# Kernel tuning notes

Measured on AMD Instinct MI355X. Metric: run time of the kernel, lower is better.

Reference implementation:

```python
import jax, jax.numpy as jnp
import numpy as np

# Fixed problem sizes (match input_specs): B graphs of N points each, kNN with K neighbors.
B, N, K = 32, 2048, 20
F_IN, H, C = 3, 64, 40
BN = B * N
E = BN * K


def mlp(x, w1, b1, w2, b2):
    # PyG MLP([in, H, H]) with plain last layer: Lin -> ReLU -> Lin
    return jax.nn.relu(x @ w1 + b1) @ w2 + b2


def edge_conv(x, src, dst, w1, b1, w2, b2):
    # EdgeConv message for edge j->i: MLP(cat[x_i, x_j - x_i]); aggr='max' at target i.
    xi = x[dst]                      # [E, F]
    xj = x[src]                      # [E, F]
    msg = mlp(jnp.concatenate([xi, xj - xi], axis=-1), w1, b1, w2, b2)  # [E, H]
    out = jax.ops.segment_max(msg, dst, num_segments=x.shape[0])        # [BN, H]
    # nodes with no incoming edges: -inf -> 0 (torch_scatter max fill behavior)
    return jnp.where(jnp.isfinite(out), out, jnp.zeros((), out.dtype))


def dynamic_edge_conv(x, w1, b1, w2, b2):
    # Rebuild kNN graph from current features within each graph, then EdgeConv(max).
    xb = x.reshape(B, N, -1)                                   # [B, N, H]
    sq = jnp.sum(xb * xb, axis=-1)                             # [B, N]
    # squared euclidean distances [B, N, N]
    d = sq[:, :, None] - 2.0 * jnp.einsum('bnh,bmh->bnm', xb, xb) + sq[:, None, :]
    _, idx = jax.lax.top_k(-d, K)                              # [B, N, K] nearest (incl. self)
    xj = jax.vmap(lambda xg, ig: xg[ig])(xb, idx)              # [B, N, K, H]
    xi = jnp.broadcast_to(xb[:, :, None, :], xj.shape)         # [B, N, K, H]
    msg = mlp(jnp.concatenate([xi, xj - xi], axis=-1), w1, b1, w2, b2)  # [B, N, K, H]
    return jnp.max(msg, axis=2).reshape(BN, -1)                # exactly K msgs per node


def _lin_init(key, fan_in, fan_out):
    k1, k2 = jax.random.split(key)
    s = 1.0 / np.sqrt(fan_in)
    w = jax.random.uniform(k1, (fan_in, fan_out), jnp.float32, -s, s)
    b = jax.random.uniform(k2, (fan_out,), jnp.float32, -s, s)
    return w, b


def setup_inputs() -> dict:
    key = jax.random.key(0)
    ks = jax.random.split(key, 10)
    x = jax.random.normal(ks[0], (BN, F_IN), jnp.float32)
    edge_index = jax.random.randint(ks[1], (2, E), 0, BN, jnp.int64)
    batch = (jnp.arange(BN) // N).astype(jnp.int64)
    c1_w1, c1_b1 = _lin_init(ks[2], 2 * F_IN, H)
    c1_w2, c1_b2 = _lin_init(ks[3], H, H)
    d1_w1, d1_b1 = _lin_init(ks[4], 2 * H, H)
    d1_w2, d1_b2 = _lin_init(ks[5], H, H)
    d2_w1, d2_b1 = _lin_init(ks[6], 2 * H, H)
    d2_w2, d2_b2 = _lin_init(ks[7], H, H)
    lin_w, lin_b = _lin_init(ks[8], H, C)
    return dict(x=x, edge_index=edge_index, batch=batch,
                c1_w1=c1_w1, c1_b1=c1_b1, c1_w2=c1_w2, c1_b2=c1_b2,
                d1_w1=d1_w1, d1_b1=d1_b1, d1_w2=d1_w2, d1_b2=d1_b2,
                d2_w1=d2_w1, d2_b1=d2_b1, d2_w2=d2_w2, d2_b2=d2_b2,
                lin_w=lin_w, lin_b=lin_b)


def reference(x, edge_index, batch,
              c1_w1, c1_b1, c1_w2, c1_b2,
              d1_w1, d1_b1, d1_w2, d1_b2,
              d2_w1, d2_b1, d2_w2, d2_b2,
              lin_w, lin_b):
    # batch is assumed sorted with equal-size graphs (arange // N); kNN is done per graph.
    src, dst = edge_index[0], edge_index[1]
    h = edge_conv(x, src, dst, c1_w1, c1_b1, c1_w2, c1_b2)
    h = dynamic_edge_conv(jax.nn.elu(h), d1_w1, d1_b1, d1_w2, d1_b2)
    h = dynamic_edge_conv(jax.nn.elu(h), d2_w1, d2_b1, d2_w2, d2_b2)
    return h @ lin_w + lin_b
```

## Files before the change

### kernel.cpp

```cpp
#include <hip/hip_runtime.h>
#include <math.h>

#define Bg 32
#define Ng 2048
#define Kn 20
#define BNn (Bg*Ng)
#define En (BNn*Kn)
#define Hd 64
#define Cd 40

#define KK 24
#define CAPB 7

typedef __attribute__((ext_vector_type(8))) short bf16x8;
typedef __attribute__((ext_vector_type(4))) float f32x4;

__device__ __forceinline__ unsigned enc_f32(float f){
  unsigned u = __float_as_uint(f);
  return ((int)u < 0) ? ~u : (u | 0x80000000u);
}

__global__ void prep_w_kernel(const float* __restrict__ w1c, const float* __restrict__ w1d1,
                              const float* __restrict__ w1d2,
                              float* __restrict__ wpq0, float* __restrict__ wpq1,
                              float* __restrict__ wpq2){
  int t = blockIdx.x*256 + threadIdx.x;
  if (t < 3*128){
    int d = t >> 7, l = t & 127;
    wpq0[t] = (l < 64) ? (w1c[d*64 + l] - w1c[(d+3)*64 + l]) : w1c[(d+3)*64 + (l-64)];
  }
  if (t < 64*128){
    int d = t >> 7, l = t & 127;
    wpq1[t] = (l < 64) ? (w1d1[d*64 + l] - w1d1[(d+64)*64 + l]) : w1d1[(d+64)*64 + (l-64)];
    wpq2[t] = (l < 64) ? (w1d2[d*64 + l] - w1d2[(d+64)*64 + l]) : w1d2[(d+64)*64 + (l-64)];
  }
}

__global__ void zero_kernel(int* __restrict__ p){
  p[blockIdx.x*256 + threadIdx.x] = 0;
}

__global__ void init_enc_kernel(unsigned int* __restrict__ enc){
  enc[blockIdx.x*256 + threadIdx.x] = 0x007FFFFFu;
}

template<int D>
__global__ __launch_bounds__(128) void gemm_pq_kernel(const float* __restrict__ x,
                               const float* __restrict__ w,
                               float* __restrict__ P, float* __restrict__ Q){
  __shared__ float xs[8*D];
  int l = threadIdx.x;
  int node0 = blockIdx.x*8;
  float wc[D];
  #pragma unroll
  for (int d=0; d<D; d++) wc[d] = w[d*128 + l];
  for (int i=l; i < 8*D; i += 128) xs[i] = x[(size_t)node0*D + i];
  __syncthreads();
  #pragma unroll
  for (int n=0; n<8; n++){
    float s = 0.f;
    #pragma unroll
    for (int d=0; d<D; d++) s = fmaf(xs[n*D+d], wc[d], s);
    int node = node0 + n;
    if (l < 64) P[(size_t)node*64 + l] = s;
    else        Q[(size_t)node*64 + (l-64)] = s;
  }
}

__global__ __launch_bounds__(256) void sqxb_kernel(const float* __restrict__ x,
        float* __restrict__ sq, unsigned short* __restrict__ xb){
  int t = blockIdx.x*256 + threadIdx.x;
  int node = t >> 6, l = t & 63;
  float v = x[t];
  unsigned u = __float_as_uint(v);
  xb[t] = (unsigned short)((u + 0x7FFFu + ((u >> 16) & 1u)) >> 16);
  float s = v*v;
  #pragma unroll
  for (int o=32; o; o>>=1) s += __shfl_xor(s, o, 64);
  if (l == 0) sq[node] = s;
}

__global__ __launch_bounds__(256) void decode_sqxb_kernel(const unsigned int* __restrict__ enc,
        const float* __restrict__ b2, float* __restrict__ x,
        float* __restrict__ sq, unsigned short* __restrict__ xb){
  int t = blockIdx.x*256 + threadIdx.x;
  int node = t >> 6, l = t & 63;
  unsigned int e = enc[t];
  unsigned int bits = (e & 0x80000000u) ? (e ^ 0x80000000u) : ~e;
  float f = __uint_as_float(bits);
  if (isfinite(f)) f += b2[l]; else f = 0.f;
  f = f > 0.f ? f : expm1f(f);
  x[t] = f;
  unsigned u = __float_as_uint(f);
  xb[t] = (unsigned short)((u + 0x7FFFu + ((u >> 16) & 1u)) >> 16);
  float s = f*f;
  #pragma unroll
  for (int o=32; o; o>>=1) s += __shfl_xor(s, o, 64);
  if (l == 0) sq[node] = s;
}

__global__ void count_kernel(const int* __restrict__ ei, int* __restrict__ deg){
  int e = blockIdx.x*256 + threadIdx.x;
  atomicAdd(&deg[ei[En + e]], 1);
}

__global__ __launch_bounds__(1024) void scan_kernel(const int* __restrict__ deg,
        int* __restrict__ rowptr, int* __restrict__ cursor){
  __shared__ int ps[1024];
  int t = threadIdx.x;
  int base = t*64;
  int s = 0;
  for (int k=0;k<64;k++) s += deg[base+k];
  ps[t] = s; __syncthreads();
  for (int off=1; off<1024; off<<=1){
    int v = (t>=off) ? ps[t-off] : 0;
    __syncthreads();
    ps[t] += v;
    __syncthreads();
  }
  int run = (t>0) ? ps[t-1] : 0;
  for (int k=0;k<64;k++){
    rowptr[base+k] = run; cursor[base+k] = run;
    run += deg[base+k];
  }
  if (t==1023) rowptr[BNn] = run;
}

__global__ void scatter_kernel(const int* __restrict__ ei, int* __restrict__ cursor,
                               int* __restrict__ csrc, int* __restrict__ enid){
  int e = blockIdx.x*256 + threadIdx.x;
  int s = ei[e], d = ei[En + e];
  int pos = atomicAdd(&cursor[d], 1);
  csrc[pos] = s;
  enid[pos] = d;
}

#define FMA8(av, r) \
  acc[r][0]=fmaf(av,b0.x,acc[r][0]); acc[r][1]=fmaf(av,b0.y,acc[r][1]); \
  acc[r][2]=fmaf(av,b0.z,acc[r][2]); acc[r][3]=fmaf(av,b0.w,acc[r][3]); \
  acc[r][4]=fmaf(av,b1v.x,acc[r][4]); acc[r][5]=fmaf(av,b1v.y,acc[r][5]); \
  acc[r][6]=fmaf(av,b1v.z,acc[r][6]); acc[r][7]=fmaf(av,b1v.w,acc[r][7]);

__global__ __launch_bounds__(256,3) void econv_gemm_kernel(
    const int* __restrict__ csrc, const int* __restrict__ enid,
    const float* __restrict__ P, const float* __restrict__ Q,
    const float* __restrict__ b1, const float* __restrict__ w2,
    unsigned int* __restrict__ enc){
  __shared__ __align__(16) float As[32*256];
  __shared__ __align__(16) float Ws[64*64];
  __shared__ int eids[256];
  int tid = threadIdx.x;
  int e0 = ((blockIdx.x & 7)*640 + (blockIdx.x >> 3))*256;
  int e = e0 + tid;
  int j = csrc[e];
  int i = enid[e];
  eids[tid] = i;
  const float* Pr = P + (size_t)i*Hd;
  const float* Qr = Q + (size_t)j*Hd;
  #pragma unroll
  for (int c=0;c<16;c++) Ws[c*256 + tid] = w2[c*256 + tid];

  int m0 = tid >> 3, n0 = tid & 7;
  float acc[8][8];
  #pragma unroll
  for (int a=0;a<8;a++)
    #pragma unroll
    for (int b=0;b<8;b++) acc[a][b]=0.f;

  #pragma unroll 1
  for (int kh=0; kh<2; kh++){
    __syncthreads();
    #pragma unroll
    for (int c=0;c<8;c++){
      int k = kh*32 + 4*c;
      float4 q4 = *(const float4*)(Qr + k);
      float4 pk = *(const float4*)(Pr + k);
      float4 b4 = *(const float4*)(b1 + k);
      As[(4*c+0)*256 + tid] = fmaxf(pk.x+q4.x+b4.x, 0.f);
      As[(4*c+1)*256 + tid] = fmaxf(pk.y+q4.y+b4.y, 0.f);
      As[(4*c+2)*256 + tid] = fmaxf(pk.z+q4.z+b4.z, 0.f);
      As[(4*c+3)*256 + tid] = fmaxf(pk.w+q4.w+b4.w, 0.f);
    }
    __syncthreads();
    #pragma unroll 4
    for (int kk=0; kk<32; kk++){
      int k = kh*32 + kk;
      float4 a0 = *(const float4*)&As[kk*256 + 8*m0];
      float4 a1 = *(const float4*)&As[kk*256 + 8*m0 + 4];
      float4 b0 = *(const float4*)&Ws[k*64 + 8*n0];
      float4 b1v = *(const float4*)&Ws[k*64 + 8*n0 + 4];
      FMA8(a0.x, 0) FMA8(a0.y, 1) FMA8(a0.z, 2) FMA8(a0.w, 3)
      FMA8(a1.x, 4) FMA8(a1.y, 5) FMA8(a1.z, 6) FMA8(a1.w, 7)
    }
  }
  unsigned* lmax = (unsigned*)As;
  int nfirst = eids[0];
  __syncthreads();
  for (int z = tid; z < 32*65; z += 256) lmax[z] = 0u;
  __syncthreads();
  {
    int rbase = 8*m0;
    int cur = eids[rbase];
    float vmax[8];
    #pragma unroll
    for (int b=0;b<8;b++) vmax[b] = -INFINITY;
    #pragma unroll
    for (int a=0;a<8;a++){
      int id = eids[rbase + a];
      if (id != cur){
        int lid = cur - nfirst;
        if (lid < 32){
          #pragma unroll
          for (int b=0;b<8;b++) atomicMax(&lmax[lid*65 + 8*n0 + b], enc_f32(vmax[b]));
        } else {
          #pragma unroll
          for (int b=0;b<8;b++) atomicMax(&enc[(size_t)cur*Hd + 8*n0 + b], enc_f32(vmax[b]));
        }
        #pragma unroll
        for (int b=0;b<8;b++) vmax[b] = -INFINITY;
        cur = id;
      }
      #pragma unroll
      for (int b=0;b<8;b++) vmax[b] = fmaxf(vmax[b], acc[a][b]);
    }
    int lid = cur - nfirst;
    if (lid < 32){
      #pragma unroll
      for (int b=0;b<8;b++) atomicMax(&lmax[lid*65 + 8*n0 + b], enc_f32(vmax[b]));
    } else {
      #pragma unroll
      for (int b=0;b<8;b++) atomicMax(&enc[(size_t)cur*Hd + 8*n0 + b], enc_f32(vmax[b]));
    }
  }
  __syncthreads();
  {
    int ch = tid & 63;
    for (int lid = tid >> 6; lid < 32; lid += 4){
      unsigned v = lmax[lid*65 + ch];
      if (v) atomicMax(&enc[(size_t)(nfirst + lid)*Hd + ch], v);
    }
  }
}

__device__ __forceinline__ void ins24(unsigned (&kb)[KK], unsigned key){
  #pragma unroll
  for (int p=KK-1; p>0; p--){
    unsigned ins = (key < kb[p]) ? key : kb[p];
    kb[p] = (key < kb[p-1]) ? kb[p-1] : ins;
  }
  kb[0] = (key < kb[0]) ? key : kb[0];
}

#define KNN_FLUSH() do { \
  _Pragma("unroll 1") \
  for (int c=0;c<CAPB;c++){ \
    if (!__any(c < cnt)) break; \
    unsigned kf = (c < cnt) ? kc[c][tid] : 0xFFFFFFFFu; \
    ins24(kb, kf); \
  } \
  cnt = 0; kbLast = kb[KK-1]; \
} while(0)

#define KNN_TRY(key) do { unsigned kk_ = (key); \
  if (kk_ < kbLast){ kc[cnt][tid] = kk_; cnt++; } } while(0)

#define SWZ16(base, row, stridep2, byteoff) \
  ((unsigned short*)((char*)(base) + ((((row) << (stridep2)) + (byteoff)) ^ (((row) & 7) << 4))))

__global__ __launch_bounds__(256,4) void knn_kernel(
    const unsigned short* __restrict__ xb, const float* __restrict__ sq,
    unsigned short* __restrict__ cand){
  __shared__ __align__(16) unsigned short xrb[64*64];
  __shared__ __align__(16) unsigned short xjb[128*64];
  __shared__ __align__(16) unsigned short Dt[64*128];
  unsigned (*kc)[256] = (unsigned(*)[256])xrb;
  float* sqs = (float*)((char*)xrb + 7168);

  int tid = threadIdx.x;
  int lane = tid & 63, w = tid >> 6;
  int bid = ((blockIdx.x & 7) << 7) | (blockIdx.x >> 3);
  int g  = bid >> 5;
  int r0 = (bid & 31) * 64;
  const unsigned short* xbg = xb + (size_t)g*Ng*Hd;
  const float* sg = sq + (size_t)g*Ng;

  int q = w;
  int prow = lane;
  int rw = w*16;

  {
    int r = tid >> 2, cb = (tid & 3) * 32;
    const uint4* src = (const uint4*)(xbg + (size_t)(r0 + r)*Hd + (tid & 3)*16);
    uint4 a = src[0], b = src[1];
    *(uint4*)SWZ16(xrb, r, 7, cb)      = a;
    *(uint4*)SWZ16(xrb, r, 7, cb + 16) = b;
  }
  __syncthreads();
  bf16x8 A0, A1;
  {
    int arow = rw + (lane & 15);
    A0 = *(const bf16x8*)SWZ16(xrb, arow, 7,      (lane>>4)*16);
    A1 = *(const bf16x8*)SWZ16(xrb, arow, 7, 64 + (lane>>4)*16);
  }
  __syncthreads();
  {
    int jr = tid >> 1, half = tid & 1;
    int jloc = (jr >> 5)*512 + (jr & 31);
    const uint4* src = (const uint4*)(xbg + (size_t)jloc*Hd + half*32);
    uint4 a = src[0], b = src[1], c2 = src[2], d2 = src[3];
    *(uint4*)SWZ16(xjb, jr, 7, half*64 +  0) = a;
    *(uint4*)SWZ16(xjb, jr, 7, half*64 + 16) = b;
    *(uint4*)SWZ16(xjb, jr, 7, half*64 + 32) = c2;
    *(uint4*)SWZ16(xjb, jr, 7, half*64 + 48) = d2;
    if (tid < 128) sqs[tid] = sg[(tid>>5)*512 + (tid&31)];
  }

  unsigned kb[KK];
  #pragma unroll
  for (int t=0;t<KK;t++) kb[t] = 0xFFFFFFFFu;
  unsigned kbLast = 0xFFFFFFFFu;
  int cnt = 0;

  __syncthreads();

  #pragma unroll 1
  for (int it = 0; it < 16; it++){
    uint4 pf0, pf1, pf2, pf3; float psq = 0.f;
    int itn = it + 1;
    int jr = tid >> 1, half = tid & 1;
    if (itn < 16){
      int jloc = (jr >> 5)*512 + itn*32 + (jr & 31);
      const uint4* src = (const uint4*)(xbg + (size_t)jloc*Hd + half*32);
      pf0 = src[0]; pf1 = src[1]; pf2 = src[2]; pf3 = src[3];
      if (tid < 128) psq = sg[(tid>>5)*512 + itn*32 + (tid&31)];
    }
    #pragma unroll
    for (int jb = 0; jb < 8; jb++){
      int brow = jb*16 + (lane & 15);
      bf16x8 B0 = *(const bf16x8*)SWZ16(xjb, brow, 7,      (lane>>4)*16);
      bf16x8 B1 = *(const bf16x8*)SWZ16(xjb, brow, 7, 64 + (lane>>4)*16);
      f32x4 acc = {0.f, 0.f, 0.f, 0.f};
      acc = __builtin_amdgcn_mfma_f32_16x16x32_bf16(A0, B0, acc, 0, 0, 0);
      acc = __builtin_amdgcn_mfma_f32_16x16x32_bf16(A1, B1, acc, 0, 0, 0);
      int col = jb*16 + (lane & 15);
      float sqv = sqs[col];
      int rbase = rw + (lane>>4)*4;
      #pragma unroll
      for (int v=0; v<4; v++){
        float f = fmaf(acc[v], -2.f, sqv);
        unsigned u = __float_as_uint(f);
        unsigned t2 = ((unsigned)((int)u >> 31)) | 0x8000u;
        *SWZ16(Dt, rbase + v, 8, col*2) = (unsigned short)((u >> 16) ^ t2);
      }
    }
    __syncthreads();
    int jbase0 = q*512 + it*32;
    {
      const char* dbase = (const char*)Dt + (prow << 8);
      unsigned m = (prow & 7) << 4;
      #pragma unroll
      for (int r4=0; r4<4; r4++){
        uint4 dv = *(const uint4*)(dbase + ((unsigned)(q*64 + r4*16) ^ m));
        int cb = jbase0 + r4*8;
        KNN_TRY((dv.x << 16) + (unsigned)(cb + 0));
        KNN_TRY((dv.x & 0xFFFF0000u) | (unsigned)(cb + 1));
        KNN_TRY((dv.y << 16) + (unsigned)(cb + 2));
        KNN_TRY((dv.y & 0xFFFF0000u) | (unsigned)(cb + 3));
        if (__any(cnt >= 4)) KNN_FLUSH();
        KNN_TRY((dv.z << 16) + (unsigned)(cb + 4));
        KNN_TRY((dv.z & 0xFFFF0000u) | (unsigned)(cb + 5));
        KNN_TRY((dv.w << 16) + (unsigned)(cb + 6));
        KNN_TRY((dv.w & 0xFFFF0000u) | (unsigned)(cb + 7));
        if (__any(cnt >= 4)) KNN_FLUSH();
      }
    }
    if (itn < 16){
      *(uint4*)SWZ16(xjb, jr, 7, half*64 +  0) = pf0;
      *(uint4*)SWZ16(xjb, jr, 7, half*64 + 16) = pf1;
      *(uint4*)SWZ16(xjb, jr, 7, half*64 + 32) = pf2;
      *(uint4*)SWZ16(xjb, jr, 7, half*64 + 48) = pf3;
      if (tid < 128) sqs[tid] = psq;
    }
    __syncthreads();
  }
  KNN_FLUSH();
  size_t base = (size_t)(g*Ng + r0 + prow)*96 + q*24;
  #pragma unroll
  for (int t=0;t<KK;t++)
    cand[base + t] = (unsigned short)(kb[t] & 2047u);
}

#define RR_REDUCE(BB, HH) do { \
  int c = (2*pp + HH)*16 + cg; \
  int j = js[2*pp + HH]; \
  float dot = 0.f, sqj = 0.f; \
  _Pragma("unroll") \
  for (int it2=0; it2<4; it2++){ \
    float4 b = BB[it2]; \
    float4 a = xc[it2]; \
    dot = fmaf(a.x, b.x, dot); dot = fmaf(a.y, b.y, dot); \
    dot = fmaf(a.z, b.z, dot); dot = fmaf(a.w, b.w, dot); \
    sqj = fmaf(b.x, b.x, sqj); sqj = fmaf(b.y, b.y, sqj); \
    sqj = fmaf(b.z, b.z, sqj); sqj = fmaf(b.w, b.w, sqj); \
  } \
  dot += __shfl_xor(dot, 1, 64); dot += __shfl_xor(dot, 2, 64); \
  sqj += __shfl_xor(sqj, 1, 64); sqj += __shfl_xor(sqj, 2, 64); \
  if (chunk == 0){ \
    float dist = fmaf(dot, -2.f, sqj); \
    ks[w][c] = ((unsigned long long)enc_f32(dist) << 32) | (unsigned)j; \
  } \
} while(0)

__global__ __launch_bounds__(256) void rerank_kernel(const float* __restrict__ x,
        const unsigned short* __restrict__ cand, int* __restrict__ idx){
  __shared__ __align__(16) unsigned long long ks[4][96];
  int tid = threadIdx.x;
  int lane = tid & 63, w = tid >> 6;
  int bid = ((blockIdx.x & 7) << 11) | (blockIdx.x >> 3);
  int row = bid*4 + w;
  int g = row >> 11;
  const float* xg = x + (size_t)g*Ng*Hd;
  int chunk = lane & 3;
  int cg = lane >> 2;
  const float* xr = x + (size_t)row*Hd;
  float4 xc[4];
  #pragma unroll
  for (int it2=0; it2<4; it2++) xc[it2] = *(const float4*)(xr + 16*it2 + 4*chunk);

  int js[6];
  #pragma unroll
  for (int p=0; p<6; p++) js[p] = cand[(size_t)row*96 + p*16 + cg];

  #pragma unroll 1
  for (int pp=0; pp<3; pp++){
    const float* xj0 = xg + (size_t)js[2*pp]*Hd;
    const float* xj1 = xg + (size_t)js[2*pp+1]*Hd;
    float4 bb0[4], bb1[4];
    #pragma unroll
    for (int it2=0; it2<4; it2++){
      bb0[it2] = *(const float4*)(xj0 + 16*it2 + 4*chunk);
      bb1[it2] = *(const float4*)(xj1 + 16*it2 + 4*chunk);
    }
    RR_REDUCE(bb0, 0);
    RR_REDUCE(bb1, 1);
  }
  __syncthreads();
  unsigned long long k0 = ks[w][lane];
  unsigned long long k1 = (lane < 32) ? ks[w][64 + lane] : ~0ULL;
  int r0 = 0, r1 = 0;
  #pragma unroll
  for (int c=0;c<96;c+=2){
    unsigned long long a = ks[w][c], b = ks[w][c+1];
    r0 += (a < k0) + (b < k0);
    r1 += (a < k1) + (b < k1);
  }
  if (r0 < Kn) idx[(size_t)row*Kn + r0] = g*Ng + (int)(k0 & 2047ULL);
  if (lane < 32 && r1 < Kn) idx[(size_t)row*Kn + r1] = g*Ng + (int)(k1 & 2047ULL);
}

__global__ __launch_bounds__(256,3) void emsg_kernel(
    const int* __restrict__ srcl,
    const float* __restrict__ P, const float* __restrict__ Q,
    const float* __restrict__ b1, const float* __restrict__ w2,
    unsigned int* __restrict__ enc){
  __shared__ __align__(16) char smem[49152];
  float* As = (float*)smem;
  float* Ws = (float*)(smem + 32768);
  float* p0 = (float*)smem;
  float* p1 = (float*)(smem + 64*33*4);
  int tid = threadIdx.x;
  int e0 = ((blockIdx.x & 7)*640 + (blockIdx.x >> 3))*256;
  int e = e0 + tid;
  int i = e / Kn;
  int j = srcl[e];
  const float* Pr = P + (size_t)i*Hd;
  const float* Qr = Q + (size_t)j*Hd;
  #pragma unroll
  for (int c=0;c<16;c++) Ws[c*256 + tid] = w2[c*256 + tid];

  int m0 = tid >> 3, n0 = tid & 7;
  float acc[8][8];
  #pragma unroll
  for (int a=0;a<8;a++)
    #pragma unroll
    for (int b=0;b<8;b++) acc[a][b]=0.f;

  #pragma unroll 1
  for (int kh=0; kh<2; kh++){
    __syncthreads();
    #pragma unroll
    for (int c=0;c<8;c++){
      int k = kh*32 + 4*c;
      float4 q4 = *(const float4*)(Qr + k);
      float4 pk = *(const float4*)(Pr + k);
      float4 b4 = *(const float4*)(b1 + k);
      As[(4*c+0)*256 + tid] = fmaxf(pk.x+q4.x+b4.x, 0.f);
      As[(4*c+1)*256 + tid] = fmaxf(pk.y+q4.y+b4.y, 0.f);
      As[(4*c+2)*256 + tid] = fmaxf(pk.z+q4.z+b4.z, 0.f);
      As[(4*c+3)*256 + tid] = fmaxf(pk.w+q4.w+b4.w, 0.f);
    }
    __syncthreads();
    #pragma unroll 4
    for (int kk=0; kk<32; kk++){
      int k = kh*32 + kk;
      float4 a0 = *(const float4*)&As[kk*256 + 8*m0];
      float4 a1 = *(const float4*)&As[kk*256 + 8*m0 + 4];
      float4 b0 = *(const float4*)&Ws[k*64 + 8*n0];
      float4 b1v = *(const float4*)&Ws[k*64 + 8*n0 + 4];
      FMA8(a0.x, 0) FMA8(a0.y, 1) FMA8(a0.z, 2) FMA8(a0.w, 3)
      FMA8(a1.x, 4) FMA8(a1.y, 5) FMA8(a1.z, 6) FMA8(a1.w, 7)
    }
  }
  int ebase = e0 + 8*m0;
  int nd0 = ebase / Kn;
  int split = (nd0+1)*Kn - ebase; if (split > 8) split = 8;
  float s0[8], s1[8];
  #pragma unroll
  for (int b=0;b<8;b++){ s0[b] = -INFINITY; s1[b] = -INFINITY; }
  #pragma unroll
  for (int a=0;a<8;a++)
    #pragma unroll
    for (int b=0;b<8;b++){
      if (a < split) s0[b] = fmaxf(s0[b], acc[a][b]);
      else           s1[b] = fmaxf(s1[b], acc[a][b]);
    }
  __syncthreads();
  #pragma unroll
  for (int b=0;b<8;b++){
    p0[(8*n0+b)*33 + m0] = s0[b];
    p1[(8*n0+b)*33 + m0] = s1[b];
  }
  __syncthreads();
  int nfirst = e0 / Kn;
  int ncnt = (e0 + 255) / Kn - nfirst + 1;
  int ch = tid & 63;
  for (int ln = tid >> 6; ln < ncnt; ln += 4){
    int nd = nfirst + ln;
    int glo = nd*Kn;      if (glo < e0)     glo = e0;
    int ghi = nd*Kn + Kn; if (ghi > e0+256) ghi = e0+256;
    int mlo = (glo - e0) >> 3, mhi = (ghi - 1 - e0) >> 3;
    float v = -INFINITY;
    for (int mm = mlo; mm <= mhi; mm++){
      int bn = (e0 + 8*mm) / Kn;
      if (bn == nd)     v = fmaxf(v, p0[ch*33 + mm]);
      if (bn + 1 == nd) v = fmaxf(v, p1[ch*33 + mm]);
    }
    atomicMax(&enc[(size_t)nd*Hd + ch], enc_f32(v));
  }
}

__global__ __launch_bounds__(256) void decode_kernel(const unsigned int* __restrict__ enc,
         const float* __restrict__ b2, float* __restrict__ x){
  int t = blockIdx.x*256 + threadIdx.x;
  unsigned int e = enc[t];
  unsigned int bits = (e & 0x80000000u) ? (e ^ 0x80000000u) : ~e;
  float f = __uint_as_float(bits);
  if (isfinite(f)) f += b2[t & 63]; else f = 0.f;
  x[t] = f;
}

__global__ __launch_bounds__(64) void final_kernel(const float* __restrict__ h,
        const float* __restrict__ w, const float* __restrict__ bias,
        float* __restrict__ out){
  __shared__ float xs[Hd];
  int c = threadIdx.x;
  float wc[Hd];
  float bc = 0.f;
  if (c < Cd){
    #pragma unroll
    for (int d=0; d<Hd; d++) wc[d] = w[d*Cd + c];
    bc = bias[c];
  }
  for (int i = blockIdx.x; i < BNn; i += gridDim.x){
    __syncthreads();
    xs[c] = h[(size_t)i*Hd + c];
    __syncthreads();
    if (c < Cd){
      float s = bc;
      #pragma unroll
      for (int d=0; d<Hd; d++) s = fmaf(xs[d], wc[d], s);
      out[(size_t)i*Cd + c] = s;
    }
  }
}

extern "C" void kernel_launch(void* const* d_in, const int* in_sizes, int n_in,
                              void* d_out, int out_size, void* d_ws, size_t ws_size,
                              hipStream_t stream){
  const float* x0   = (const float*)d_in[0];
  const int*   ei   = (const int*)d_in[1];
  const float* c1w1 = (const float*)d_in[3];
  const float* c1b1 = (const float*)d_in[4];
  const float* c1w2 = (const float*)d_in[5];
  const float* c1b2 = (const float*)d_in[6];
  const float* d1w1 = (const float*)d_in[7];
  const float* d1b1 = (const float*)d_in[8];
  const float* d1w2 = (const float*)d_in[9];
  const float* d1b2 = (const float*)d_in[10];
  const float* d2w1 = (const float*)d_in[11];
  const float* d2b1 = (const float*)d_in[12];
  const float* d2w2 = (const float*)d_in[13];
  const float* d2b2 = (const float*)d_in[14];
  const float* linw = (const float*)d_in[15];
  const float* linb = (const float*)d_in[16];
  float* out = (float*)d_out;

  char* ws = (char*)d_ws;
  size_t off = 0;
  auto alloc = [&](size_t bytes)->char*{
    char* p = ws + off; off += (bytes + 255) & ~(size_t)255; return p;
  };
  float*        X    = (float*)alloc(sizeof(float)*(size_t)BNn*Hd);
  float*        P    = (float*)alloc(sizeof(float)*(size_t)BNn*Hd);
  float*        Q    = (float*)alloc(sizeof(float)*(size_t)BNn*Hd);
  float*        H2   = (float*)alloc(sizeof(float)*(size_t)BNn*Hd);
  unsigned int* ENC  = (unsigned int*)alloc(sizeof(unsigned)*(size_t)BNn*Hd);
  int*          SHRD = (int*)alloc(sizeof(int)*(size_t)En);
  int*          DEG  = (int*)alloc(sizeof(int)*BNn);
  int*          RPTR = (int*)alloc(sizeof(int)*(BNn+1));
  int*          CUR  = (int*)alloc(sizeof(int)*BNn);
  float*        SQ   = (float*)alloc(sizeof(float)*BNn);
  float*        WPQ0 = (float*)alloc(sizeof(float)*3*128);
  float*        WPQ1 = (float*)alloc(sizeof(float)*64*128);
  float*        WPQ2 = (float*)alloc(sizeof(float)*64*128);
  int*            CSRC = SHRD;
  int*            IDX  = SHRD;
  int*            ENID = (int*)H2;
  unsigned short* XB   = (unsigned short*)H2;
  unsigned short* CAND = (unsigned short*)ENC;
  (void)ws_size; (void)in_sizes; (void)n_in; (void)out_size;

  prep_w_kernel<<<32, 256, 0, stream>>>(c1w1, d1w1, d2w1, WPQ0, WPQ1, WPQ2);
  zero_kernel<<<BNn/256, 256, 0, stream>>>(DEG);
  count_kernel<<<En/256, 256, 0, stream>>>(ei, DEG);
  gemm_pq_kernel<3><<<BNn/8, 128, 0, stream>>>(x0, WPQ0, P, Q);
  scan_kernel<<<1, 1024, 0, stream>>>(DEG, RPTR, CUR);
  scatter_kernel<<<En/256, 256, 0, stream>>>(ei, CUR, CSRC, ENID);
  init_enc_kernel<<<BNn*Hd/256, 256, 0, stream>>>(ENC);
  econv_gemm_kernel<<<En/256, 256, 0, stream>>>(CSRC, ENID, P, Q, c1b1, c1w2, ENC);
  decode_sqxb_kernel<<<BNn*Hd/256, 256, 0, stream>>>(ENC, c1b2, X, SQ, XB);

  gemm_pq_kernel<64><<<BNn/8, 128, 0, stream>>>(X, WPQ1, P, Q);
  knn_kernel<<<Bg*32, 256, 0, stream>>>(XB, SQ, CAND);
  rerank_kernel<<<BNn/4, 256, 0, stream>>>(X, CAND, IDX);
  init_enc_kernel<<<BNn*Hd/256, 256, 0, stream>>>(ENC);
  emsg_kernel<<<En/256, 256, 0, stream>>>(IDX, P, Q, d1b1, d1w2, ENC);
  decode_sqxb_kernel<<<BNn*Hd/256, 256, 0, stream>>>(ENC, d1b2, X, SQ, XB);

  gemm_pq_kernel<64><<<BNn/8, 128, 0, stream>>>(X, WPQ2, P, Q);
  knn_kernel<<<Bg*32, 256, 0, stream>>>(XB, SQ, CAND);
  rerank_kernel<<<BNn/4, 256, 0, stream>>>(X, CAND, IDX);
  init_enc_kernel<<<BNn*Hd/256, 256, 0, stream>>>(ENC);
  emsg_kernel<<<En/256, 256, 0, stream>>>(IDX, P, Q, d2b1, d2w2, ENC);
  decode_kernel<<<BNn*Hd/256, 256, 0, stream>>>(ENC, d2b2, H2);

  final_kernel<<<8192, 64, 0, stream>>>(H2, linw, linb, out);
}
```

Baseline: 1.434 ms.

## Split kNN rows across thread halves with 32-row tiles and merge top-K lists

The kNN kernel now handles 32 query rows per block instead of 64, with twice as many blocks. It also splits each row's candidate scan across two thread halves that alternate iterations, then merges the two sorted top-24 lists before writing candidates. Shared memory is shrunk and launch bounds raised to allow more resident blocks, aiming to increase occupancy and shorten the serial per-thread selection chain. The cost is twice as many loop iterations with more barriers, plus an extra merge step and shared-memory staging at the end.

After: 1.708 ms. +19.1%, slower.

```diff
diff --git a/kernel.cpp b/kernel.cpp
--- a/kernel.cpp
+++ b/kernel.cpp
@@ -267,52 +267,41 @@
 #define SWZ16(base, row, stridep2, byteoff) \
   ((unsigned short*)((char*)(base) + ((((row) << (stridep2)) + (byteoff)) ^ (((row) & 7) << 4))))
 
-__global__ __launch_bounds__(256,4) void knn_kernel(
+__global__ __launch_bounds__(256,8) void knn_kernel(
     const unsigned short* __restrict__ xb, const float* __restrict__ sq,
     unsigned short* __restrict__ cand){
-  __shared__ __align__(16) unsigned short xrb[64*64];
-  __shared__ __align__(16) unsigned short xjb[128*64];
-  __shared__ __align__(16) unsigned short Dt[64*128];
-  unsigned (*kc)[256] = (unsigned(*)[256])xrb;
-  float* sqs = (float*)((char*)xrb + 7168);
+  __shared__ __align__(16) char smem[19712];
+  unsigned short* xjb = (unsigned short*)smem;
+  unsigned short* Dt  = (unsigned short*)(smem + 8192);
+  unsigned (*kc)[256] = (unsigned(*)[256])(smem + 12288);
+  float* sqs = (float*)(smem + 19456);
+  unsigned* mgb = (unsigned*)smem;
 
   int tid = threadIdx.x;
   int lane = tid & 63, w = tid >> 6;
-  int bid = ((blockIdx.x & 7) << 7) | (blockIdx.x >> 3);
-  int g  = bid >> 5;
-  int r0 = (bid & 31) * 64;
+  int bid = ((blockIdx.x & 7) << 8) | (blockIdx.x >> 3);
+  int g  = bid >> 6;
+  int r0 = (bid & 63) * 32;
   const unsigned short* xbg = xb + (size_t)g*Ng*Hd;
   const float* sg = sq + (size_t)g*Ng;
 
-  int q = w;
-  int prow = lane;
-  int rw = w*16;
+  int r = tid & 31;
+  int q = (tid >> 5) & 3;
+  int h = tid >> 7;
+  int mrow = (w & 1) * 16;
+  int cbase = (w >> 1) * 32;
+
+  bf16x8 A0 = *(const bf16x8*)(xbg + (size_t)(r0 + mrow + (lane & 15))*Hd + (lane>>4)*8);
+  bf16x8 A1 = *(const bf16x8*)(xbg + (size_t)(r0 + mrow + (lane & 15))*Hd + 32 + (lane>>4)*8);
 
   {
-    int r = tid >> 2, cb = (tid & 3) * 32;
-    const uint4* src = (const uint4*)(xbg + (size_t)(r0 + r)*Hd + (tid & 3)*16);
+    int jr = tid >> 2, seg = tid & 3;
+    int jloc = (jr >> 4)*512 + (jr & 15);
+    const uint4* src = (const uint4*)(xbg + (size_t)jloc*Hd + seg*16);
     uint4 a = src[0], b = src[1];
-    *(uint4*)SWZ16(xrb, r, 7, cb)      = a;
-    *(uint4*)SWZ16(xrb, r, 7, cb + 16) = b;
-  }
-  __syncthreads();
-  bf16x8 A0, A1;
-  {
-    int arow = rw + (lane & 15);
-    A0 = *(const bf16x8*)SWZ16(xrb, arow, 7,      (lane>>4)*16);
-    A1 = *(const bf16x8*)SWZ16(xrb, arow, 7, 64 + (lane>>4)*16);
-  }
-  __syncthreads();
-  {
-    int jr = tid >> 1, half = tid & 1;
-    int jloc = (jr >> 5)*512 + (jr & 31);
-    const uint4* src = (const uint4*)(xbg + (size_t)jloc*Hd + half*32);
-    uint4 a = src[0], b = src[1], c2 = src[2], d2 = src[3];
-    *(uint4*)SWZ16(xjb, jr, 7, half*64 +  0) = a;
-    *(uint4*)SWZ16(xjb, jr, 7, half*64 + 16) = b;
-    *(uint4*)SWZ16(xjb, jr, 7, half*64 + 32) = c2;
-    *(uint4*)SWZ16(xjb, jr, 7, half*64 + 48) = d2;
-    if (tid < 128) sqs[tid] = sg[(tid>>5)*512 + (tid&31)];
+    *(uint4*)SWZ16(xjb, jr, 7, seg*32)      = a;
+    *(uint4*)SWZ16(xjb, jr, 7, seg*32 + 16) = b;
+    if (tid < 64) sqs[tid] = sg[(tid>>4)*512 + (tid & 15)];
   }
 
   unsigned kb[KK];
@@ -324,44 +313,45 @@
   __syncthreads();
 
   #pragma unroll 1
-  for (int it = 0; it < 16; it++){
-    uint4 pf0, pf1, pf2, pf3; float psq = 0.f;
+  for (int it = 0; it < 32; it++){
+    uint4 pf0, pf1; float psq = 0.f;
     int itn = it + 1;
-    int jr = tid >> 1, half = tid & 1;
-    if (itn < 16){
-      int jloc = (jr >> 5)*512 + itn*32 + (jr & 31);
-      const uint4* src = (const uint4*)(xbg + (size_t)jloc*Hd + half*32);
-      pf0 = src[0]; pf1 = src[1]; pf2 = src[2]; pf3 = src[3];
-      if (tid < 128) psq = sg[(tid>>5)*512 + itn*32 + (tid&31)];
-    }
-    #pragma unroll
-    for (int jb = 0; jb < 8; jb++){
-      int brow = jb*16 + (lane & 15);
-      bf16x8 B0 = *(const bf16x8*)SWZ16(xjb, brow, 7,      (lane>>4)*16);
-      bf16x8 B1 = *(const bf16x8*)SWZ16(xjb, brow, 7, 64 + (lane>>4)*16);
+    int jr = tid >> 2, seg = tid & 3;
+    if (itn < 32){
+      int jloc = (jr >> 4)*512 + itn*16 + (jr & 15);
+      const uint4* src = (const uint4*)(xbg + (size_t)jloc*Hd + seg*16);
+      pf0 = src[0]; pf1 = src[1];
+      if (tid < 64) psq = sg[(tid>>4)*512 + itn*16 + (tid & 15)];
+    }
+    #pragma unroll
+    for (int jb = 0; jb < 2; jb++){
+      int cl = cbase + jb*16 + (lane & 15);
+      bf16x8 B0 = *(const bf16x8*)SWZ16(xjb, cl, 7,      (lane>>4)*16);
+      bf16x8 B1 = *(const bf16x8*)SWZ16(xjb, cl, 7, 64 + (lane>>4)*16);
       f32x4 acc = {0.f, 0.f, 0.f, 0.f};
       acc = __builtin_amdgcn_mfma_f32_16x16x32_bf16(A0, B0, acc, 0, 0, 0);
       acc = __builtin_amdgcn_mfma_f32_16x16x32_bf16(A1, B1, acc, 0, 0, 0);
-      int col = jb*16 + (lane & 15);
-      float sqv = sqs[col];
-      int rbase = rw + (lane>>4)*4;
+      float sqv = sqs[cl];
+      int rbase = mrow + (lane>>4)*4;
       #pragma unroll
       for (int v=0; v<4; v++){
         float f = fmaf(acc[v], -2.f, sqv);
         unsigned u = __float_as_uint(f);
         unsigned t2 = ((unsigned)((int)u >> 31)) | 0x8000u;
-        *SWZ16(Dt, rbase + v, 8, col*2) = (unsigned short)((u >> 16) ^ t2);
+        *SWZ16(Dt, rbase + v, 7, cl*2) = (unsigned short)((u >> 16) ^ t2);
       }
     }
     __syncthreads();
-    int jbase0 = q*512 + it*32;
-    {
-      const char* dbase = (const char*)Dt + (prow << 8);
-      unsigned m = (prow & 7) << 4;
+    if ((it & 1) == h){
+      int cb0 = q*512 + it*16;
+      const char* dbase = (const char*)Dt + (r << 7);
+      unsigned m = (r & 7) << 4;
+      uint4 dv0 = *(const uint4*)(dbase + ((unsigned)(q*32) ^ m));
+      uint4 dv1 = *(const uint4*)(dbase + ((unsigned)(q*32 + 16) ^ m));
       #pragma unroll
-      for (int r4=0; r4<4; r4++){
-        uint4 dv = *(const uint4*)(dbase + ((unsigned)(q*64 + r4*16) ^ m));
-        int cb = jbase0 + r4*8;
+      for (int r4=0; r4<2; r4++){
+        uint4 dv = r4 ? dv1 : dv0;
+        int cb = cb0 + r4*8;
         KNN_TRY((dv.x << 16) + (unsigned)(cb + 0));
         KNN_TRY((dv.x & 0xFFFF0000u) | (unsigned)(cb + 1));
         KNN_TRY((dv.y << 16) + (unsigned)(cb + 2));
@@ -374,20 +364,40 @@
         if (__any(cnt >= 4)) KNN_FLUSH();
       }
     }
-    if (itn < 16){
-      *(uint4*)SWZ16(xjb, jr, 7, half*64 +  0) = pf0;
-      *(uint4*)SWZ16(xjb, jr, 7, half*64 + 16) = pf1;
-      *(uint4*)SWZ16(xjb, jr, 7, half*64 + 32) = pf2;
-      *(uint4*)SWZ16(xjb, jr, 7, half*64 + 48) = pf3;
-      if (tid < 128) sqs[tid] = psq;
+    if (itn < 32){
+      *(uint4*)SWZ16(xjb, jr, 7, seg*32)      = pf0;
+      *(uint4*)SWZ16(xjb, jr, 7, seg*32 + 16) = pf1;
+      if (tid < 64) sqs[tid] = psq;
     }
     __syncthreads();
   }
   KNN_FLUSH();
-  size_t base = (size_t)(g*Ng + r0 + prow)*96 + q*24;
-  #pragma unroll
-  for (int t=0;t<KK;t++)
-    cand[base + t] = (unsigned short)(kb[t] & 2047u);
+
+  __syncthreads();
+  int sl = tid & 127;
+  if (h == 1){
+    #pragma unroll
+    for (int t=0;t<KK;t++) mgb[sl*24 + t] = kb[t];
+  }
+  __syncthreads();
+  if (h == 0){
+    size_t base = (size_t)(g*Ng + r0 + r)*96 + q*24;
+    int j = 0;
+    unsigned bv = mgb[sl*24];
+    #pragma unroll
+    for (int i=0;i<KK;i++){
+      unsigned av = kb[i];
+      #pragma unroll 1
+      while (j < KK && bv < av){
+        int rk = i + j;
+        if (rk < KK) cand[base + rk] = (unsigned short)(bv & 2047u);
+        j++;
+        bv = (j < KK) ? mgb[sl*24 + j] : 0xFFFFFFFFu;
+      }
+      int rk = i + j;
+      if (rk < KK) cand[base + rk] = (unsigned short)(av & 2047u);
+    }
+  }
 }
 
 #define RR_REDUCE(BB, HH) do { \
@@ -641,14 +651,14 @@
   decode_sqxb_kernel<<<BNn*Hd/256, 256, 0, stream>>>(ENC, c1b2, X, SQ, XB);
 
   gemm_pq_kernel<64><<<BNn/8, 128, 0, stream>>>(X, WPQ1, P, Q);
-  knn_kernel<<<Bg*32, 256, 0, stream>>>(XB, SQ, CAND);
+  knn_kernel<<<Bg*64, 256, 0, stream>>>(XB, SQ, CAND);
   rerank_kernel<<<BNn/4, 256, 0, stream>>>(X, CAND, IDX);
   init_enc_kernel<<<BNn*Hd/256, 256, 0, stream>>>(ENC);
   emsg_kernel<<<En/256, 256, 0, stream>>>(IDX, P, Q, d1b1, d1w2, ENC);
   decode_sqxb_kernel<<<BNn*Hd/256, 256, 0, stream>>>(ENC, d1b2, X, SQ, XB);
 
   gemm_pq_kernel<64><<<BNn/8, 128, 0, stream>>>(X, WPQ2, P, Q);
-  knn_kernel<<<Bg*32, 256, 0, stream>>>(XB, SQ, CAND);
+  knn_kernel<<<Bg*64, 256, 0, stream>>>(XB, SQ, CAND);
   rerank_kernel<<<BNn/4, 256, 0, stream>>>(X, CAND, IDX);
   init_enc_kernel<<<BNn*Hd/256, 256, 0, stream>>>(ENC);
   emsg_kernel<<<En/256, 256, 0, stream>>>(IDX, P, Q, d2b1, d2w2, ENC);
```
